# Kernel tuning notes

Measured on AMD Instinct MI355X. Metric: run time of the kernel, lower is better.

Reference implementation:

```python
import jax, jax.numpy as jnp
import numpy as np

B, L, D, N_ITEMS = 512, 100, 128, 100000
ALPHA = 0.3


def setup_inputs() -> dict:
    key = jax.random.key(0)
    ks = jax.random.split(key, 10)
    x = jax.random.randint(ks[0], (B, L), 0, N_ITEMS, dtype=jnp.int32)
    attn_mask = jnp.ones((B, L), dtype=bool)  # unused by forward (parity with torch signature)
    emb = jax.random.normal(ks[1], (N_ITEMS, D), dtype=jnp.float32) * 0.02
    emb = emb.at[0].set(0.0)  # padding_idx=0 row is zeros
    s = 1.0 / np.sqrt(D)
    W_in = jax.random.uniform(ks[2], (D, D), minval=-s, maxval=s, dtype=jnp.float32)
    W_out = jax.random.uniform(ks[3], (D, D), minval=-s, maxval=s, dtype=jnp.float32)
    w_ih = jax.random.uniform(ks[4], (3 * D, D), minval=-s, maxval=s, dtype=jnp.float32)
    w_hh = jax.random.uniform(ks[5], (3 * D, D), minval=-s, maxval=s, dtype=jnp.float32)
    b_ih = jax.random.uniform(ks[6], (3 * D,), minval=-s, maxval=s, dtype=jnp.float32)
    b_hh = jax.random.uniform(ks[7], (3 * D,), minval=-s, maxval=s, dtype=jnp.float32)
    sr = 1.0 / np.sqrt(3 * D)
    W_read = jax.random.uniform(ks[8], (D, 3 * D), minval=-sr, maxval=sr, dtype=jnp.float32)
    b_read = jax.random.uniform(ks[9], (D,), minval=-sr, maxval=sr, dtype=jnp.float32)
    return dict(x=x, attn_mask=attn_mask, emb=emb, W_in=W_in, W_out=W_out,
                w_ih=w_ih, w_hh=w_hh, b_ih=b_ih, b_hh=b_hh, W_read=W_read, b_read=b_read)


def _forward(x, emb, W_in, W_out, w_ih, w_hh, b_ih, b_hh, W_read, b_read):
    n_items, d = emb.shape
    seq_len = x.shape[1]
    BIG = n_items  # sentinel > any item id
    NEG = -1e9

    def per_sample(seq):
        valid = seq != 0
        cnt = valid.sum()
        # --- torch.unique(nonzero, return_inverse=True) via sort + dedup ---
        s = jnp.where(valid, seq, BIG)
        ss = jnp.sort(s)
        prev = jnp.concatenate([jnp.full((1,), -1, ss.dtype), ss[:-1]])
        is_first = (ss != prev) & (ss != BIG)
        n_nodes = is_first.sum()
        rank = jnp.cumsum(is_first) - 1
        nodes_s = jnp.full((seq_len,), BIG, ss.dtype).at[
            jnp.where(is_first, rank, seq_len)].set(ss, mode='drop')  # sorted unique ids, BIG-padded
        node_mask = jnp.arange(seq_len) < n_nodes
        nodes = jnp.where(node_mask, nodes_s, 0)  # pad slots -> item 0 (zero emb row)
        inv = jnp.searchsorted(nodes_s, s)  # inverse indices for valid positions
        # compact nonzero items preserving order (for consecutive-pair edges)
        pos = jnp.cumsum(valid) - 1
        cidx = jnp.where(valid, pos, seq_len)
        compact_inv = jnp.zeros((seq_len,), inv.dtype).at[cidx].set(inv, mode='drop')
        compact_seq = jnp.zeros((seq_len,), seq.dtype).at[cidx].set(seq, mode='drop')
        last_tok = compact_seq[jnp.maximum(cnt - 1, 0)]
        src, dst = compact_inv[:-1], compact_inv[1:]
        edge_mask = jnp.arange(seq_len - 1) < cnt - 1
        # --- message passing: index_add + degree normalize ---
        H0 = emb[nodes]  # [L, d]
        Hin = H0 @ W_in.T
        Hout = H0 @ W_out.T
        dst_safe = jnp.where(edge_mask, dst, seq_len)
        agg = jnp.zeros((seq_len, d), H0.dtype).at[dst_safe].add(
            jnp.where(edge_mask[:, None], Hout[src], 0.0), mode='drop')
        deg = jnp.zeros((seq_len,), H0.dtype).at[dst_safe].add(1.0, mode='drop')
        deg = jnp.maximum(deg, 1.0)
        xin = Hin + agg / deg[:, None]
        # --- GRUCell(xin, H0), torch gate order (r, z, n) ---
        gi = xin @ w_ih.T + b_ih
        gh = H0 @ w_hh.T + b_hh
        gi_r, gi_z, gi_n = jnp.split(gi, 3, axis=-1)
        gh_r, gh_z, gh_n = jnp.split(gh, 3, axis=-1)
        r = jax.nn.sigmoid(gi_r + gh_r)
        z = jax.nn.sigmoid(gi_z + gh_z)
        nct = jnp.tanh(gi_n + r * gh_n)
        H = (1.0 - z) * nct + z * H0
        H = jnp.where(node_mask[:, None], H, 0.0)  # drop padded node slots
        # --- attention readout anchored at last item ---
        li = jnp.clip(jnp.searchsorted(nodes_s, last_tok), 0, seq_len - 1)
        h_last = H[li]
        scores = jnp.where(node_mask, H @ h_last, NEG)
        att = jax.nn.softmax(scores)
        local = att @ H
        gvec = jnp.zeros((d,), H.dtype)  # cooc is None -> zeros_like(local)
        h_read = jnp.tanh(W_read @ jnp.concatenate([h_last, local, ALPHA * gvec]) + b_read)
        row = h_read @ emb.T  # tied output weights
        default = jnp.full((n_items,), NEG, row.dtype).at[0].set(0.0)
        return jnp.where(cnt >= 2, row, default)

    return jax.vmap(per_sample)(x)


def reference(x, attn_mask, emb, W_in, W_out, w_ih, w_hh, b_ih, b_hh, W_read, b_read):
    return _forward(x, emb, W_in, W_out, w_ih, w_hh, b_ih, b_hh, W_read, b_read)
```

## Files before the change

kernel.cpp:

```cpp
#include <hip/hip_runtime.h>
#include <math.h>

#define BATCH 512
#define SEQL  100
#define DIM   128
#define NITEMS 100000
#define NEGV  -1000000000.0f

#define OFF_WREADT 131072
#define OFF_HREAD  180224
#define OFF_DEG    245760
#define OFF_XIN    296960
#define OFF_HOUT   6850560
#define OFF_EPACK_F (OFF_XIN + 131072)
#define OFF_NODES_I 13404160
#define OFF_SRC_I   13455360
#define OFF_DST_I   13506048
#define OFF_INFO_I  13556736
#define OFF_WPACK_F 13558784

typedef __attribute__((ext_vector_type(8))) short bf16x8;
typedef __attribute__((ext_vector_type(4))) short s16x4;
typedef __attribute__((ext_vector_type(4))) float f32x4;

__device__ __forceinline__ unsigned short bf16_rne(float x) {
  unsigned int u = __float_as_uint(x);
  unsigned int r = u + 0x7FFFu + ((u >> 16) & 1u);
  return (unsigned short)(r >> 16);
}
__device__ __forceinline__ float bf16_to_f(unsigned short h) {
  return __uint_as_float(((unsigned int)h) << 16);
}

__global__ void k_prep(const float* __restrict__ w_ih, const float* __restrict__ w_hh,
                       const float* __restrict__ W_in, const float* __restrict__ W_out,
                       const float* __restrict__ W_read, float* __restrict__ ws,
                       unsigned short* __restrict__ wpack) {
  int idx = blockIdx.x * 256 + threadIdx.x;
  if (idx < 98304) {
    int mat = idx / 49152, rem = idx % 49152;
    int n = rem / 128, k = rem % 128;
    float v = (mat ? w_hh : w_ih)[rem];
    unsigned short hi = bf16_rne(v);
    unsigned short lo = bf16_rne(v - bf16_to_f(hi));
    int nt = n >> 4, nn = n & 15, c = k >> 5, quad = (k >> 3) & 3, j = k & 7;
    int lane = quad * 16 + nn;
    size_t base = ((size_t)((mat * 24 + nt) * 4 + c)) * 1024 + (size_t)lane * 8 + j;
    wpack[base] = hi;
    wpack[base + 512] = lo;
  }
  if (idx < 49152) {
    int i = idx / 384, jj = idx % 384;
    ws[OFF_WREADT + jj * 128 + i] = W_read[idx];
  }
  if (idx < 32768) {
    int mat = idx >> 14, rem = idx & 16383;
    int n = rem >> 7, k = rem & 127;
    float v = (mat ? W_out : W_in)[rem];
    unsigned short hi = bf16_rne(v);
    unsigned short lo = bf16_rne(v - bf16_to_f(hi));
    int nt = n >> 4, nn = n & 15, c = k >> 5, quad = (k >> 3) & 3, j = k & 7;
    int lane = quad * 16 + nn;
    size_t base = ((size_t)((mat * 8 + nt) * 4 + c)) * 1024 + (size_t)lane * 8 + j;
    unsigned short* wpack2 = (unsigned short*)ws;
    wpack2[base] = hi;
    wpack2[base + 512] = lo;
  }
}

__global__ void k_build(const int* __restrict__ x, int* __restrict__ nodes,
                        float* __restrict__ deg, int* __restrict__ esrc,
                        int* __restrict__ edst, int* __restrict__ info) {
  int b = blockIdx.x, tid = threadIdx.x;
  __shared__ int sseq[SEQL];
  __shared__ int sfo[SEQL];
  __shared__ unsigned char sisf[SEQL];
  __shared__ int srank[SEQL];
  __shared__ int spos[SEQL];
  __shared__ int scinv[SEQL];
  __shared__ float sdeg[SEQL];
  __shared__ int s_nn, s_cnt;

  if (tid < SEQL) sseq[tid] = x[b * SEQL + tid];
  __syncthreads();
  int t = (tid < SEQL) ? sseq[tid] : 0;
  bool valid = (tid < SEQL) && (t != 0);
  int f = tid;
  if (valid) {
    for (int j = 0; j < tid; ++j) {
      if (sseq[j] == t) { f = j; break; }
    }
  }
  if (tid < SEQL) {
    sfo[tid] = f;
    sisf[tid] = (valid && f == tid) ? 1 : 0;
    sdeg[tid] = 0.f;
  }
  __syncthreads();
  if (tid == 0) {
    int nn = 0, c = 0;
    for (int i = 0; i < SEQL; ++i) {
      srank[i] = nn; nn += sisf[i];
      spos[i] = c;  c += (sseq[i] != 0) ? 1 : 0;
    }
    s_nn = nn; s_cnt = c;
  }
  __syncthreads();
  int nn = s_nn, cnt = s_cnt;
  if (valid) scinv[spos[tid]] = srank[sfo[tid]];
  __syncthreads();
  if (tid < SEQL) {
    if (sisf[tid]) nodes[b * SEQL + srank[tid]] = t;
    if (tid >= nn) nodes[b * SEQL + tid] = 0;
  }
  __syncthreads();
  if (tid == 0) {
    int ec = (cnt >= 2) ? cnt - 1 : 0;
    for (int e = 0; e < ec; ++e) {
      int s = scinv[e], dnode = scinv[e + 1];
      esrc[b * 99 + e] = s;
      edst[b * 99 + e] = dnode;
      sdeg[dnode] += 1.f;
    }
    info[b * 4 + 0] = ec;
    info[b * 4 + 1] = (cnt >= 1) ? scinv[cnt - 1] : 0;
    info[b * 4 + 2] = (cnt >= 2) ? 1 : 0;
    info[b * 4 + 3] = nn;
  }
  __syncthreads();
  if (tid < SEQL) deg[b * SEQL + tid] = fmaxf(sdeg[tid], 1.f);
}

#define GPAD 136
__global__ __launch_bounds__(128) void k_gemm_inout(
    const float* __restrict__ emb, const unsigned short* __restrict__ wpack2,
    const int* __restrict__ nodes, float* __restrict__ xin, float* __restrict__ hout) {
  __shared__ unsigned short Hhi[32 * GPAD];
  __shared__ unsigned short Hlo[32 * GPAD];
  int tid = threadIdx.x;
  int rowbase = blockIdx.x * 32;
  const float4* emb4 = (const float4*)emb;
  for (int e = tid; e < 32 * 32; e += 128) {
    int r = e >> 5, c4 = e & 31;
    int tok = nodes[rowbase + r];
    float4 hv = emb4[(size_t)tok * 32 + c4];
    int base = r * GPAD + c4 * 4;
    float hs[4] = {hv.x, hv.y, hv.z, hv.w};
    #pragma unroll
    for (int q = 0; q < 4; ++q) {
      unsigned short hh = bf16_rne(hs[q]);
      Hhi[base + q] = hh;
      Hlo[base + q] = bf16_rne(hs[q] - bf16_to_f(hh));
    }
  }
  __syncthreads();
  int wave = tid >> 6, lane = tid & 63;
  int quad = lane >> 4, nIdx = lane & 15;
  int mrow = wave * 16 + nIdx;
  bf16x8 aH[4], aL[4];
  #pragma unroll
  for (int c = 0; c < 4; ++c) {
    int off = mrow * GPAD + c * 32 + quad * 8;
    aH[c] = *(const bf16x8*)&Hhi[off];
    aL[c] = *(const bf16x8*)&Hlo[off];
  }
  for (int t = 0; t < 8; ++t) {
    f32x4 accI = (f32x4){0.f, 0.f, 0.f, 0.f};
    f32x4 accO = (f32x4){0.f, 0.f, 0.f, 0.f};
    #pragma unroll
    for (int c = 0; c < 4; ++c) {
      size_t bi = ((size_t)((0 * 8 + t) * 4 + c)) * 1024 + (size_t)lane * 8;
      size_t bo = ((size_t)((1 * 8 + t) * 4 + c)) * 1024 + (size_t)lane * 8;
      bf16x8 BiH = *(const bf16x8*)&wpack2[bi];
      bf16x8 BiL = *(const bf16x8*)&wpack2[bi + 512];
      bf16x8 BoH = *(const bf16x8*)&wpack2[bo];
      bf16x8 BoL = *(const bf16x8*)&wpack2[bo + 512];
      accI = __builtin_amdgcn_mfma_f32_16x16x32_bf16(aH[c], BiH, accI, 0, 0, 0);
      accO = __builtin_amdgcn_mfma_f32_16x16x32_bf16(aH[c], BoH, accO, 0, 0, 0);
      accI = __builtin_amdgcn_mfma_f32_16x16x32_bf16(aL[c], BiH, accI, 0, 0, 0);
      accO = __builtin_amdgcn_mfma_f32_16x16x32_bf16(aL[c], BoH, accO, 0, 0, 0);
      accI = __builtin_amdgcn_mfma_f32_16x16x32_bf16(aH[c], BiL, accI, 0, 0, 0);
      accO = __builtin_amdgcn_mfma_f32_16x16x32_bf16(aH[c], BoL, accO, 0, 0, 0);
    }
    int j = t * 16 + nIdx;
    #pragma unroll
    for (int i = 0; i < 4; ++i) {
      size_t row = (size_t)(rowbase + wave * 16 + quad * 4 + i);
      xin[row * 128 + j]  = accI[i];
      hout[row * 128 + j] = accO[i];
    }
  }
}

__global__ void k_scatter(const float* __restrict__ hout, float* __restrict__ xin,
                          const float* __restrict__ deg, const int* __restrict__ esrc,
                          const int* __restrict__ edst, const int* __restrict__ info) {
  int b = blockIdx.x, k = threadIdx.x;
  __shared__ float agg[SEQL * DIM];
  for (int n = 0; n < SEQL; ++n) agg[n * DIM + k] = 0.f;
  int ec = info[b * 4 + 0];
  for (int e = 0; e < ec; ++e) {
    int s = esrc[b * 99 + e], dn = edst[b * 99 + e];
    agg[dn * DIM + k] += hout[((size_t)(b * SEQL + s)) * DIM + k];
  }
  for (int n = 0; n < SEQL; ++n) {
    float dg = deg[b * SEQL + n];
    size_t idx = ((size_t)(b * SEQL + n)) * DIM + k;
    xin[idx] += agg[n * DIM + k] / dg;
  }
}

__global__ __launch_bounds__(128) void k_gru(
    const float* __restrict__ emb, const int* __restrict__ nodes,
    const unsigned short* __restrict__ wpack, const float* __restrict__ xin,
    const float* __restrict__ b_ih, const float* __restrict__ b_hh,
    const int* __restrict__ info, float* __restrict__ Hbuf) {
  __shared__ unsigned short Xhi[32 * GPAD];
  __shared__ unsigned short Xlo[32 * GPAD];
  __shared__ unsigned short Hhi[32 * GPAD];
  __shared__ unsigned short Hlo[32 * GPAD];
  int tid = threadIdx.x;
  int rowbase = blockIdx.x * 32;
  const float4* emb4 = (const float4*)emb;
  const float4* xin4 = (const float4*)xin;
  for (int e = tid; e < 32 * 32; e += 128) {
    int r = e >> 5, c4 = e & 31;
    int row = rowbase + r;
    float4 xv = xin4[(size_t)row * 32 + c4];
    int tok = nodes[row];
    float4 hv = emb4[(size_t)tok * 32 + c4];
    int base = r * GPAD + c4 * 4;
    float xs[4] = {xv.x, xv.y, xv.z, xv.w};
    float hs[4] = {hv.x, hv.y, hv.z, hv.w};
    #pragma unroll
    for (int q = 0; q < 4; ++q) {
      unsigned short xh = bf16_rne(xs[q]);
      Xhi[base + q] = xh; Xlo[base + q] = bf16_rne(xs[q] - bf16_to_f(xh));
      unsigned short hh = bf16_rne(hs[q]);
      Hhi[base + q] = hh; Hlo[base + q] = bf16_rne(hs[q] - bf16_to_f(hh));
    }
  }
  __syncthreads();
  int wave = tid >> 6, lane = tid & 63;
  int quad = lane >> 4, nIdx = lane & 15;
  int mrow = wave * 16 + nIdx;
  bf16x8 aXh[4], aXl[4], aHh[4], aHl[4];
  #pragma unroll
  for (int c = 0; c < 4; ++c) {
    int off = mrow * GPAD + c * 32 + quad * 8;
    aXh[c] = *(const bf16x8*)&Xhi[off];
    aXl[c] = *(const bf16x8*)&Xlo[off];
    aHh[c] = *(const bf16x8*)&Hhi[off];
    aHl[c] = *(const bf16x8*)&Hlo[off];
  }
  int grows[4]; int zm[4];
  #pragma unroll
  for (int i = 0; i < 4; ++i) {
    int grow = rowbase + wave * 16 + quad * 4 + i;
    grows[i] = grow;
    int bs = grow / SEQL;
    int n = grow - bs * SEQL;
    zm[i] = (n < info[bs * 4 + 3]) ? 1 : 0;
  }

  for (int t = 0; t < 8; ++t) {
    f32x4 acc[3][2];
    #pragma unroll
    for (int g = 0; g < 3; ++g)
      #pragma unroll
      for (int m = 0; m < 2; ++m) acc[g][m] = (f32x4){0.f, 0.f, 0.f, 0.f};

    for (int c = 0; c < 4; ++c) {
      bf16x8 Bh[3][2], Bl[3][2];
      #pragma unroll
      for (int g = 0; g < 3; ++g) {
        int nt = g * 8 + t;
        #pragma unroll
        for (int m = 0; m < 2; ++m) {
          size_t bidx = (size_t)((m * 24 + nt) * 4 + c) * 1024 + (size_t)lane * 8;
          Bh[g][m] = *(const bf16x8*)&wpack[bidx];
          Bl[g][m] = *(const bf16x8*)&wpack[bidx + 512];
        }
      }
      #pragma unroll
      for (int g = 0; g < 3; ++g) {
        acc[g][0] = __builtin_amdgcn_mfma_f32_16x16x32_bf16(aXh[c], Bh[g][0], acc[g][0], 0, 0, 0);
        acc[g][1] = __builtin_amdgcn_mfma_f32_16x16x32_bf16(aHh[c], Bh[g][1], acc[g][1], 0, 0, 0);
      }
      #pragma unroll
      for (int g = 0; g < 3; ++g) {
        acc[g][0] = __builtin_amdgcn_mfma_f32_16x16x32_bf16(aXh[c], Bl[g][0], acc[g][0], 0, 0, 0);
        acc[g][1] = __builtin_amdgcn_mfma_f32_16x16x32_bf16(aHh[c], Bl[g][1], acc[g][1], 0, 0, 0);
      }
      #pragma unroll
      for (int g = 0; g < 3; ++g) {
        acc[g][0] = __builtin_amdgcn_mfma_f32_16x16x32_bf16(aXl[c], Bh[g][0], acc[g][0], 0, 0, 0);
        acc[g][1] = __builtin_amdgcn_mfma_f32_16x16x32_bf16(aHl[c], Bh[g][1], acc[g][1], 0, 0, 0);
      }
    }
    int j = t * 16 + nIdx;
    float biR = b_ih[j],       bhR = b_hh[j];
    float biZ = b_ih[128 + j], bhZ = b_hh[128 + j];
    float biN = b_ih[256 + j], bhN = b_hh[256 + j];
    #pragma unroll
    for (int i = 0; i < 4; ++i) {
      float gr = acc[0][0][i] + biR + acc[0][1][i] + bhR;
      float gz = acc[1][0][i] + biZ + acc[1][1][i] + bhZ;
      float r = 1.f / (1.f + expf(-gr));
      float z = 1.f / (1.f + expf(-gz));
      float nct = tanhf(acc[2][0][i] + biN + r * (acc[2][1][i] + bhN));
      int lrow = wave * 16 + quad * 4 + i;
      float h0 = bf16_to_f(Hhi[lrow * GPAD + j]) + bf16_to_f(Hlo[lrow * GPAD + j]);
      float h = (1.f - z) * nct + z * h0;
      if (!zm[i]) h = 0.f;
      Hbuf[(size_t)grows[i] * 128 + j] = h;
    }
  }
}

#define HLS 129
__global__ void k_attn(const float* __restrict__ Hbuf, const float* __restrict__ ws,
                       const float* __restrict__ b_read, const int* __restrict__ info,
                       float* __restrict__ hread) {
  int b = blockIdx.x, tid = threadIdx.x;
  __shared__ float Hl[SEQL * HLS];
  __shared__ float sc[128];
  __shared__ float hl[128];
  __shared__ float att[SEQL];
  __shared__ float loc[128];
  __shared__ float redm[2], reds[2];
  int nn = info[b * 4 + 3], li = info[b * 4 + 1];
  for (int e = tid; e < SEQL * 128; e += 128) {
    int r = e >> 7, k = e & 127;
    Hl[r * HLS + k] = Hbuf[((size_t)(b * SEQL + r)) * DIM + k];
  }
  __syncthreads();
  hl[tid] = Hl[li * HLS + tid];
  __syncthreads();
  float scr = NEGV;
  if (tid < nn) {
    float s = 0.f;
    for (int k = 0; k < 128; ++k) s += Hl[tid * HLS + k] * hl[k];
    scr = s;
  }
  sc[tid] = scr;
  __syncthreads();
  float m = sc[tid];
  #pragma unroll
  for (int o = 32; o >= 1; o >>= 1) m = fmaxf(m, __shfl_xor(m, o, 64));
  if ((tid & 63) == 0) redm[tid >> 6] = m;
  __syncthreads();
  m = fmaxf(redm[0], redm[1]);
  float e = (tid < SEQL) ? expf(sc[tid] - m) : 0.f;
  float s = e;
  #pragma unroll
  for (int o = 32; o >= 1; o >>= 1) s += __shfl_xor(s, o, 64);
  if ((tid & 63) == 0) reds[tid >> 6] = s;
  __syncthreads();
  float inv = 1.f / (reds[0] + reds[1]);
  if (tid < SEQL) att[tid] = e * inv;
  __syncthreads();
  float lv = 0.f;
  for (int n = 0; n < SEQL; ++n) lv = fmaf(att[n], Hl[n * HLS + tid], lv);
  loc[tid] = lv;
  __syncthreads();
  const float* WrT = ws + OFF_WREADT;
  float acc = b_read[tid];
  for (int j = 0; j < 128; ++j) acc = fmaf(WrT[j * 128 + tid], hl[j], acc);
  for (int j = 0; j < 128; ++j) acc = fmaf(WrT[(128 + j) * 128 + tid], loc[j], acc);
  hread[b * 128 + tid] = tanhf(acc);
}

__global__ __launch_bounds__(256) void k_packA(
    const float* __restrict__ hread, unsigned short* __restrict__ apack) {
  int idx = blockIdx.x * 256 + threadIdx.x;
  if (idx >= 8192) return;
  int lane = idx & 63;
  int kc = (idx >> 6) & 3;
  int mt = idx >> 8;
  int quad = lane >> 4, rr = lane & 15;
  int row = mt * 16 + rr;
  int kbase = kc * 32 + quad * 8;
  const float4* hr4 = (const float4*)(hread + row * 128 + kbase);
  float4 v0 = hr4[0], v1 = hr4[1];
  float vs[8] = {v0.x, v0.y, v0.z, v0.w, v1.x, v1.y, v1.z, v1.w};
  bf16x8 hi, lo;
  #pragma unroll
  for (int j = 0; j < 8; ++j) {
    unsigned short h = bf16_rne(vs[j]);
    hi[j] = (short)h;
    lo[j] = (short)bf16_rne(vs[j] - bf16_to_f(h));
  }
  size_t base = ((size_t)(mt * 4 + kc) * 2) * 512 + (size_t)lane * 8;
  *(bf16x8*)&apack[base] = hi;
  *(bf16x8*)&apack[base + 512] = lo;
}

__global__ __launch_bounds__(256) void k_epack(
    const float* __restrict__ emb, unsigned short* __restrict__ epack) {
  int idx = blockIdx.x * 256 + threadIdx.x;
  int lane = idx & 63;
  int kc = (idx >> 6) & 3;
  int it = idx >> 8;
  int quad = lane >> 4, rr = lane & 15;
  int row = it * 16 + rr;
  int kbase = kc * 32 + quad * 8;
  float4 v0 = {0.f, 0.f, 0.f, 0.f}, v1 = {0.f, 0.f, 0.f, 0.f};
  if (row < NITEMS) {
    const float4* p = (const float4*)(emb + (size_t)row * 128 + kbase);
    v0 = p[0]; v1 = p[1];
  }
  float vs[8] = {v0.x, v0.y, v0.z, v0.w, v1.x, v1.y, v1.z, v1.w};
  bf16x8 hi, lo;
  #pragma unroll
  for (int j = 0; j < 8; ++j) {
    unsigned short h = bf16_rne(vs[j]);
    hi[j] = (short)h;
    lo[j] = (short)bf16_rne(vs[j] - bf16_to_f(h));
  }
  size_t base = ((size_t)(it * 4 + kc) * 2) * 512 + (size_t)lane * 8;
  *(bf16x8*)&epack[base] = hi;
  *(bf16x8*)&epack[base + 512] = lo;
}

__global__ __launch_bounds__(256) void k_out(
    const unsigned short* __restrict__ epack, const unsigned short* __restrict__ apack,
    const int* __restrict__ info, float* __restrict__ out) {
  int tid = threadIdx.x;
  int wave = tid >> 6, lane = tid & 63;
  int quad = lane >> 4, nIdx = lane & 15;
  int b0   = blockIdx.x * 128;
  int itt0 = blockIdx.y * 4;
  int btg0 = blockIdx.x * 8 + wave * 2;

  bf16x8 bh[2][4], bl[2][4];
  #pragma unroll
  for (int m2 = 0; m2 < 2; ++m2)
    #pragma unroll
    for (int kc = 0; kc < 4; ++kc) {
      size_t base = ((size_t)((btg0 + m2) * 4 + kc) * 2) * 512 + (size_t)lane * 8;
      bh[m2][kc] = *(const bf16x8*)&apack[base];
      bl[m2][kc] = *(const bf16x8*)&apack[base + 512];
    }

  f32x4 acc[4][2];
  #pragma unroll
  for (int it = 0; it < 4; ++it)
    #pragma unroll
    for (int m2 = 0; m2 < 2; ++m2) acc[it][m2] = (f32x4){0.f, 0.f, 0.f, 0.f};

  #pragma unroll
  for (int it = 0; it < 4; ++it) {
    #pragma unroll
    for (int kc = 0; kc < 4; ++kc) {
      size_t abase = ((size_t)((itt0 + it) * 4 + kc) * 2) * 512 + (size_t)lane * 8;
      bf16x8 Ah = *(const bf16x8*)&epack[abase];
      bf16x8 Al = *(const bf16x8*)&epack[abase + 512];
      acc[it][0] = __builtin_amdgcn_mfma_f32_16x16x32_bf16(Ah, bh[0][kc], acc[it][0], 0, 0, 0);
      acc[it][1] = __builtin_amdgcn_mfma_f32_16x16x32_bf16(Ah, bh[1][kc], acc[it][1], 0, 0, 0);
      acc[it][0] = __builtin_amdgcn_mfma_f32_16x16x32_bf16(Al, bh[0][kc], acc[it][0], 0, 0, 0);
      acc[it][1] = __builtin_amdgcn_mfma_f32_16x16x32_bf16(Al, bh[1][kc], acc[it][1], 0, 0, 0);
      acc[it][0] = __builtin_amdgcn_mfma_f32_16x16x32_bf16(Ah, bl[0][kc], acc[it][0], 0, 0, 0);
      acc[it][1] = __builtin_amdgcn_mfma_f32_16x16x32_bf16(Ah, bl[1][kc], acc[it][1], 0, 0, 0);
    }
  }

  #pragma unroll
  for (int m2 = 0; m2 < 2; ++m2) {
    int b = b0 + (wave * 2 + m2) * 16 + nIdx;
    int flag = info[b * 4 + 2];
    #pragma unroll
    for (int it = 0; it < 4; ++it) {
      int ib = (itt0 + it) * 16 + quad * 4;
      if (ib < NITEMS) {
        float4 v;
        if (flag) {
          v.x = acc[it][m2][0]; v.y = acc[it][m2][1];
          v.z = acc[it][m2][2]; v.w = acc[it][m2][3];
        } else {
          v.x = (ib == 0) ? 0.f : NEGV; v.y = NEGV; v.z = NEGV; v.w = NEGV;
        }
        *(float4*)&out[(size_t)b * NITEMS + ib] = v;
      }
    }
  }
}

extern "C" void kernel_launch(void* const* d_in, const int* in_sizes, int n_in,
                              void* d_out, int out_size, void* d_ws, size_t ws_size,
                              hipStream_t stream) {
  const int*   x      = (const int*)d_in[0];
  const float* emb    = (const float*)d_in[2];
  const float* W_in   = (const float*)d_in[3];
  const float* W_out  = (const float*)d_in[4];
  const float* w_ih   = (const float*)d_in[5];
  const float* w_hh   = (const float*)d_in[6];
  const float* b_ih   = (const float*)d_in[7];
  const float* b_hh   = (const float*)d_in[8];
  const float* W_read = (const float*)d_in[9];
  const float* b_read = (const float*)d_in[10];
  float* ws  = (float*)d_ws;
  int*   wsi = (int*)d_ws;
  unsigned short* wpack  = (unsigned short*)(ws + OFF_WPACK_F);
  unsigned short* wpack2 = (unsigned short*)ws;
  unsigned short* apack  = (unsigned short*)(ws + OFF_XIN);
  unsigned short* epack  = (unsigned short*)(ws + OFF_EPACK_F);
  float* out = (float*)d_out;

  k_prep<<<384, 256, 0, stream>>>(w_ih, w_hh, W_in, W_out, W_read, ws, wpack);
  k_build<<<BATCH, 128, 0, stream>>>(x, wsi + OFF_NODES_I, ws + OFF_DEG,
                                     wsi + OFF_SRC_I, wsi + OFF_DST_I, wsi + OFF_INFO_I);
  k_gemm_inout<<<1600, 128, 0, stream>>>(emb, wpack2, wsi + OFF_NODES_I,
                                         ws + OFF_XIN, ws + OFF_HOUT);
  k_scatter<<<BATCH, 128, 0, stream>>>(ws + OFF_HOUT, ws + OFF_XIN, ws + OFF_DEG,
                                       wsi + OFF_SRC_I, wsi + OFF_DST_I, wsi + OFF_INFO_I);
  k_gru<<<1600, 128, 0, stream>>>(emb, wsi + OFF_NODES_I, wpack, ws + OFF_XIN,
                                  b_ih, b_hh, wsi + OFF_INFO_I, ws + OFF_HOUT);
  k_attn<<<BATCH, 128, 0, stream>>>(ws + OFF_HOUT, ws, b_read, wsi + OFF_INFO_I,
                                    ws + OFF_HREAD);
  k_epack<<<6252, 256, 0, stream>>>(emb, epack);
  k_packA<<<32, 256, 0, stream>>>(ws + OFF_HREAD, apack);
  k_out<<<dim3(4, 1563), 256, 0, stream>>>(epack, apack, wsi + OFF_INFO_I, out);
}
```

Measured before the change: 473.5 us.

## Fuse graph build, aggregation and GRU into one per-sample kernel

Measured after the change: 827.0 us. +74.7%, slower.

```diff
diff --git a/kernel.cpp b/kernel.cpp
--- a/kernel.cpp
+++ b/kernel.cpp
@@ -7,17 +7,12 @@
 #define NITEMS 100000
 #define NEGV  -1000000000.0f
 
-#define OFF_WREADT 131072
-#define OFF_HREAD  180224
-#define OFF_DEG    245760
-#define OFF_XIN    296960
-#define OFF_HOUT   6850560
-#define OFF_EPACK_F (OFF_XIN + 131072)
-#define OFF_NODES_I 13404160
-#define OFF_SRC_I   13455360
-#define OFF_DST_I   13506048
-#define OFF_INFO_I  13556736
-#define OFF_WPACK_F 13558784
+#define OFF_WPACK_F 0
+#define OFF_WREADT  147456
+#define OFF_APACK_F 196608
+#define OFF_HBUF    262144
+#define OFF_EPACK_F 6815744
+#define OFF_INFO_I  19619840
 
 typedef __attribute__((ext_vector_type(8))) short bf16x8;
 typedef __attribute__((ext_vector_type(4))) short s16x4;
@@ -32,296 +27,262 @@
   return __uint_as_float(((unsigned int)h) << 16);
 }
 
-__global__ void k_prep(const float* __restrict__ w_ih, const float* __restrict__ w_hh,
-                       const float* __restrict__ W_in, const float* __restrict__ W_out,
-                       const float* __restrict__ W_read, float* __restrict__ ws,
-                       unsigned short* __restrict__ wpack) {
-  int idx = blockIdx.x * 256 + threadIdx.x;
-  if (idx < 98304) {
+__global__ __launch_bounds__(256) void k_pack(
+    const float* __restrict__ emb, const float* __restrict__ w_ih,
+    const float* __restrict__ w_hh, const float* __restrict__ W_in,
+    const float* __restrict__ W_out, const float* __restrict__ W_read,
+    float* __restrict__ WreadT, unsigned short* __restrict__ wpack,
+    unsigned short* __restrict__ epack) {
+  int bid = blockIdx.x, tid = threadIdx.x;
+  if (bid < 6252) {
+    int idx = bid * 256 + tid;
+    int lane = idx & 63;
+    int kc = (idx >> 6) & 3;
+    int it = idx >> 8;
+    int quad = lane >> 4, rr = lane & 15;
+    int row = it * 16 + rr;
+    int kbase = kc * 32 + quad * 8;
+    float4 v0 = {0.f, 0.f, 0.f, 0.f}, v1 = {0.f, 0.f, 0.f, 0.f};
+    if (row < NITEMS) {
+      const float4* p = (const float4*)(emb + (size_t)row * 128 + kbase);
+      v0 = p[0]; v1 = p[1];
+    }
+    float vs[8] = {v0.x, v0.y, v0.z, v0.w, v1.x, v1.y, v1.z, v1.w};
+    bf16x8 hi, lo;
+    #pragma unroll
+    for (int j = 0; j < 8; ++j) {
+      unsigned short h = bf16_rne(vs[j]);
+      hi[j] = (short)h;
+      lo[j] = (short)bf16_rne(vs[j] - bf16_to_f(h));
+    }
+    size_t base = ((size_t)(it * 4 + kc) * 2) * 512 + (size_t)lane * 8;
+    *(bf16x8*)&epack[base] = hi;
+    *(bf16x8*)&epack[base + 512] = lo;
+  } else if (bid < 6828) {
+    int idx = (bid - 6252) * 256 + tid;
     int mat = idx / 49152, rem = idx % 49152;
-    int n = rem / 128, k = rem % 128;
-    float v = (mat ? w_hh : w_ih)[rem];
+    int n = rem >> 7, k = rem & 127;
+    float v;
+    if (mat == 2) {
+      v = w_hh[rem];
+    } else {
+      const float* Wx = mat ? W_out : W_in;
+      const float* wr = w_ih + n * 128;
+      float s = 0.f;
+      for (int m = 0; m < 128; ++m) s = fmaf(wr[m], Wx[m * 128 + k], s);
+      v = s;
+    }
     unsigned short hi = bf16_rne(v);
     unsigned short lo = bf16_rne(v - bf16_to_f(hi));
-    int nt = n >> 4, nn = n & 15, c = k >> 5, quad = (k >> 3) & 3, j = k & 7;
-    int lane = quad * 16 + nn;
+    int nt = n >> 4, nn2 = n & 15, c = k >> 5, quad = (k >> 3) & 3, j = k & 7;
+    int lane = quad * 16 + nn2;
     size_t base = ((size_t)((mat * 24 + nt) * 4 + c)) * 1024 + (size_t)lane * 8 + j;
     wpack[base] = hi;
     wpack[base + 512] = lo;
-  }
-  if (idx < 49152) {
+  } else {
+    int idx = (bid - 6828) * 256 + tid;
     int i = idx / 384, jj = idx % 384;
-    ws[OFF_WREADT + jj * 128 + i] = W_read[idx];
-  }
-  if (idx < 32768) {
-    int mat = idx >> 14, rem = idx & 16383;
-    int n = rem >> 7, k = rem & 127;
-    float v = (mat ? W_out : W_in)[rem];
-    unsigned short hi = bf16_rne(v);
-    unsigned short lo = bf16_rne(v - bf16_to_f(hi));
-    int nt = n >> 4, nn = n & 15, c = k >> 5, quad = (k >> 3) & 3, j = k & 7;
-    int lane = quad * 16 + nn;
-    size_t base = ((size_t)((mat * 8 + nt) * 4 + c)) * 1024 + (size_t)lane * 8 + j;
-    unsigned short* wpack2 = (unsigned short*)ws;
-    wpack2[base] = hi;
-    wpack2[base + 512] = lo;
-  }
-}
-
-__global__ void k_build(const int* __restrict__ x, int* __restrict__ nodes,
-                        float* __restrict__ deg, int* __restrict__ esrc,
-                        int* __restrict__ edst, int* __restrict__ info) {
-  int b = blockIdx.x, tid = threadIdx.x;
+    WreadT[jj * 128 + i] = W_read[idx];
+  }
+}
+
+__global__ __launch_bounds__(512) void k_fused(
+    const int* __restrict__ x, const float* __restrict__ emb,
+    const unsigned short* __restrict__ wpack,
+    const float* __restrict__ b_ih, const float* __restrict__ b_hh,
+    int* __restrict__ info, float* __restrict__ Hbuf) {
+  __shared__ unsigned short H0s[2 * 112 * 136];
+  __shared__ float Gmem[15232];
+  __shared__ unsigned short Bst[2 * 9216];
   __shared__ int sseq[SEQL];
-  __shared__ int sfo[SEQL];
   __shared__ unsigned char sisf[SEQL];
   __shared__ int srank[SEQL];
-  __shared__ int spos[SEQL];
   __shared__ int scinv[SEQL];
-  __shared__ float sdeg[SEQL];
+  __shared__ int snodes[112];
+  __shared__ float sdeg[112];
   __shared__ int s_nn, s_cnt;
+  int b = blockIdx.x, tid = threadIdx.x;
 
   if (tid < SEQL) sseq[tid] = x[b * SEQL + tid];
+  if (tid < 112) { snodes[tid] = 0; sdeg[tid] = 0.f; }
   __syncthreads();
   int t = (tid < SEQL) ? sseq[tid] : 0;
   bool valid = (tid < SEQL) && (t != 0);
   int f = tid;
   if (valid) {
-    for (int j = 0; j < tid; ++j) {
-      if (sseq[j] == t) { f = j; break; }
-    }
-  }
+    for (int j = 0; j < tid; ++j) if (sseq[j] == t) { f = j; break; }
+  }
+  int isf = (valid && f == tid) ? 1 : 0;
+  if (tid < SEQL) sisf[tid] = (unsigned char)isf;
+  __syncthreads();
+  int rank = 0, pos = 0;
   if (tid < SEQL) {
-    sfo[tid] = f;
-    sisf[tid] = (valid && f == tid) ? 1 : 0;
-    sdeg[tid] = 0.f;
-  }
-  __syncthreads();
+    for (int i = 0; i < tid; ++i) {
+      rank += sisf[i];
+      pos += (sseq[i] != 0) ? 1 : 0;
+    }
+    srank[tid] = rank;
+    if (tid == SEQL - 1) { s_nn = rank + isf; s_cnt = pos + (valid ? 1 : 0); }
+  }
+  __syncthreads();
+  if (valid) scinv[pos] = srank[f];
+  if (isf) snodes[rank] = t;
+  __syncthreads();
+  int nn = s_nn, cnt = s_cnt;
+  int ec = (cnt >= 2) ? cnt - 1 : 0;
+  if (tid < ec) atomicAdd(&sdeg[scinv[tid + 1]], 1.f);
   if (tid == 0) {
-    int nn = 0, c = 0;
-    for (int i = 0; i < SEQL; ++i) {
-      srank[i] = nn; nn += sisf[i];
-      spos[i] = c;  c += (sseq[i] != 0) ? 1 : 0;
-    }
-    s_nn = nn; s_cnt = c;
-  }
-  __syncthreads();
-  int nn = s_nn, cnt = s_cnt;
-  if (valid) scinv[spos[tid]] = srank[sfo[tid]];
-  __syncthreads();
-  if (tid < SEQL) {
-    if (sisf[tid]) nodes[b * SEQL + srank[tid]] = t;
-    if (tid >= nn) nodes[b * SEQL + tid] = 0;
-  }
-  __syncthreads();
-  if (tid == 0) {
-    int ec = (cnt >= 2) ? cnt - 1 : 0;
-    for (int e = 0; e < ec; ++e) {
-      int s = scinv[e], dnode = scinv[e + 1];
-      esrc[b * 99 + e] = s;
-      edst[b * 99 + e] = dnode;
-      sdeg[dnode] += 1.f;
-    }
     info[b * 4 + 0] = ec;
     info[b * 4 + 1] = (cnt >= 1) ? scinv[cnt - 1] : 0;
     info[b * 4 + 2] = (cnt >= 2) ? 1 : 0;
     info[b * 4 + 3] = nn;
   }
-  __syncthreads();
-  if (tid < SEQL) deg[b * SEQL + tid] = fmaxf(sdeg[tid], 1.f);
-}
-
-#define GPAD 136
-__global__ __launch_bounds__(128) void k_gemm_inout(
-    const float* __restrict__ emb, const unsigned short* __restrict__ wpack2,
-    const int* __restrict__ nodes, float* __restrict__ xin, float* __restrict__ hout) {
-  __shared__ unsigned short Hhi[32 * GPAD];
-  __shared__ unsigned short Hlo[32 * GPAD];
-  int tid = threadIdx.x;
-  int rowbase = blockIdx.x * 32;
   const float4* emb4 = (const float4*)emb;
-  for (int e = tid; e < 32 * 32; e += 128) {
+  for (int e = tid; e < 112 * 32; e += 512) {
     int r = e >> 5, c4 = e & 31;
-    int tok = nodes[rowbase + r];
-    float4 hv = emb4[(size_t)tok * 32 + c4];
-    int base = r * GPAD + c4 * 4;
-    float hs[4] = {hv.x, hv.y, hv.z, hv.w};
+    float4 v = emb4[(size_t)snodes[r] * 32 + c4];
+    float vs[4] = {v.x, v.y, v.z, v.w};
+    s16x4 hv, lv;
     #pragma unroll
     for (int q = 0; q < 4; ++q) {
-      unsigned short hh = bf16_rne(hs[q]);
-      Hhi[base + q] = hh;
-      Hlo[base + q] = bf16_rne(hs[q] - bf16_to_f(hh));
-    }
-  }
-  __syncthreads();
-  int wave = tid >> 6, lane = tid & 63;
+      unsigned short h = bf16_rne(vs[q]);
+      hv[q] = (short)h;
+      lv[q] = (short)bf16_rne(vs[q] - bf16_to_f(h));
+    }
+    *(s16x4*)&H0s[r * 136 + c4 * 4] = hv;
+    *(s16x4*)&H0s[112 * 136 + r * 136 + c4 * 4] = lv;
+  }
+  float4* G4 = (float4*)Gmem;
+  for (int e = tid; e < 112 * 33; e += 512) G4[e] = (float4){0.f, 0.f, 0.f, 0.f};
+  __syncthreads();
+  for (int idx = tid; idx < ec * 128; idx += 512) {
+    int e = idx >> 7, k = idx & 127;
+    int src = scinv[e], dst = scinv[e + 1];
+    float v = bf16_to_f(H0s[src * 136 + k]) + bf16_to_f(H0s[112 * 136 + src * 136 + k]);
+    atomicAdd(&Gmem[dst * 132 + k], v);
+  }
+  __syncthreads();
+  float sv[28];
+  #pragma unroll
+  for (int u = 0; u < 28; ++u) {
+    int e = tid + u * 512;
+    int r = e >> 7, k = e & 127;
+    sv[u] = Gmem[r * 132 + k] * (1.f / fmaxf(sdeg[r], 1.f));
+  }
+  __syncthreads();
+  unsigned short* GdU = (unsigned short*)Gmem;
+  #pragma unroll
+  for (int u = 0; u < 28; ++u) {
+    int e = tid + u * 512;
+    int r = e >> 7, k = e & 127;
+    unsigned short hi = bf16_rne(sv[u]);
+    GdU[r * 136 + k] = hi;
+    GdU[112 * 136 + r * 136 + k] = bf16_rne(sv[u] - bf16_to_f(hi));
+  }
+  __syncthreads();
+
+  int w = tid >> 6, lane = tid & 63;
   int quad = lane >> 4, nIdx = lane & 15;
-  int mrow = wave * 16 + nIdx;
-  bf16x8 aH[4], aL[4];
-  #pragma unroll
-  for (int c = 0; c < 4; ++c) {
-    int off = mrow * GPAD + c * 32 + quad * 8;
-    aH[c] = *(const bf16x8*)&Hhi[off];
-    aL[c] = *(const bf16x8*)&Hlo[off];
-  }
-  for (int t = 0; t < 8; ++t) {
-    f32x4 accI = (f32x4){0.f, 0.f, 0.f, 0.f};
-    f32x4 accO = (f32x4){0.f, 0.f, 0.f, 0.f};
+  const uint4* wp4 = (const uint4*)wpack;
+  uint4* bst4 = (uint4*)Bst;
+
+  bf16x8 a0h[4], a0l[4], a1h[4], a1l[4];
+  if (w < 7) {
     #pragma unroll
     for (int c = 0; c < 4; ++c) {
-      size_t bi = ((size_t)((0 * 8 + t) * 4 + c)) * 1024 + (size_t)lane * 8;
-      size_t bo = ((size_t)((1 * 8 + t) * 4 + c)) * 1024 + (size_t)lane * 8;
-      bf16x8 BiH = *(const bf16x8*)&wpack2[bi];
-      bf16x8 BiL = *(const bf16x8*)&wpack2[bi + 512];
-      bf16x8 BoH = *(const bf16x8*)&wpack2[bo];
-      bf16x8 BoL = *(const bf16x8*)&wpack2[bo + 512];
-      accI = __builtin_amdgcn_mfma_f32_16x16x32_bf16(aH[c], BiH, accI, 0, 0, 0);
-      accO = __builtin_amdgcn_mfma_f32_16x16x32_bf16(aH[c], BoH, accO, 0, 0, 0);
-      accI = __builtin_amdgcn_mfma_f32_16x16x32_bf16(aL[c], BiH, accI, 0, 0, 0);
-      accO = __builtin_amdgcn_mfma_f32_16x16x32_bf16(aL[c], BoH, accO, 0, 0, 0);
-      accI = __builtin_amdgcn_mfma_f32_16x16x32_bf16(aH[c], BiL, accI, 0, 0, 0);
-      accO = __builtin_amdgcn_mfma_f32_16x16x32_bf16(aH[c], BoL, accO, 0, 0, 0);
-    }
-    int j = t * 16 + nIdx;
-    #pragma unroll
-    for (int i = 0; i < 4; ++i) {
-      size_t row = (size_t)(rowbase + wave * 16 + quad * 4 + i);
-      xin[row * 128 + j]  = accI[i];
-      hout[row * 128 + j] = accO[i];
-    }
-  }
-}
-
-__global__ void k_scatter(const float* __restrict__ hout, float* __restrict__ xin,
-                          const float* __restrict__ deg, const int* __restrict__ esrc,
-                          const int* __restrict__ edst, const int* __restrict__ info) {
-  int b = blockIdx.x, k = threadIdx.x;
-  __shared__ float agg[SEQL * DIM];
-  for (int n = 0; n < SEQL; ++n) agg[n * DIM + k] = 0.f;
-  int ec = info[b * 4 + 0];
-  for (int e = 0; e < ec; ++e) {
-    int s = esrc[b * 99 + e], dn = edst[b * 99 + e];
-    agg[dn * DIM + k] += hout[((size_t)(b * SEQL + s)) * DIM + k];
-  }
-  for (int n = 0; n < SEQL; ++n) {
-    float dg = deg[b * SEQL + n];
-    size_t idx = ((size_t)(b * SEQL + n)) * DIM + k;
-    xin[idx] += agg[n * DIM + k] / dg;
-  }
-}
-
-__global__ __launch_bounds__(128) void k_gru(
-    const float* __restrict__ emb, const int* __restrict__ nodes,
-    const unsigned short* __restrict__ wpack, const float* __restrict__ xin,
-    const float* __restrict__ b_ih, const float* __restrict__ b_hh,
-    const int* __restrict__ info, float* __restrict__ Hbuf) {
-  __shared__ unsigned short Xhi[32 * GPAD];
-  __shared__ unsigned short Xlo[32 * GPAD];
-  __shared__ unsigned short Hhi[32 * GPAD];
-  __shared__ unsigned short Hlo[32 * GPAD];
-  int tid = threadIdx.x;
-  int rowbase = blockIdx.x * 32;
-  const float4* emb4 = (const float4*)emb;
-  const float4* xin4 = (const float4*)xin;
-  for (int e = tid; e < 32 * 32; e += 128) {
-    int r = e >> 5, c4 = e & 31;
-    int row = rowbase + r;
-    float4 xv = xin4[(size_t)row * 32 + c4];
-    int tok = nodes[row];
-    float4 hv = emb4[(size_t)tok * 32 + c4];
-    int base = r * GPAD + c4 * 4;
-    float xs[4] = {xv.x, xv.y, xv.z, xv.w};
-    float hs[4] = {hv.x, hv.y, hv.z, hv.w};
-    #pragma unroll
-    for (int q = 0; q < 4; ++q) {
-      unsigned short xh = bf16_rne(xs[q]);
-      Xhi[base + q] = xh; Xlo[base + q] = bf16_rne(xs[q] - bf16_to_f(xh));
-      unsigned short hh = bf16_rne(hs[q]);
-      Hhi[base + q] = hh; Hlo[base + q] = bf16_rne(hs[q] - bf16_to_f(hh));
-    }
-  }
-  __syncthreads();
-  int wave = tid >> 6, lane = tid & 63;
-  int quad = lane >> 4, nIdx = lane & 15;
-  int mrow = wave * 16 + nIdx;
-  bf16x8 aXh[4], aXl[4], aHh[4], aHl[4];
-  #pragma unroll
-  for (int c = 0; c < 4; ++c) {
-    int off = mrow * GPAD + c * 32 + quad * 8;
-    aXh[c] = *(const bf16x8*)&Xhi[off];
-    aXl[c] = *(const bf16x8*)&Xlo[off];
-    aHh[c] = *(const bf16x8*)&Hhi[off];
-    aHl[c] = *(const bf16x8*)&Hlo[off];
-  }
-  int grows[4]; int zm[4];
-  #pragma unroll
-  for (int i = 0; i < 4; ++i) {
-    int grow = rowbase + wave * 16 + quad * 4 + i;
-    grows[i] = grow;
-    int bs = grow / SEQL;
-    int n = grow - bs * SEQL;
-    zm[i] = (n < info[bs * 4 + 3]) ? 1 : 0;
-  }
-
-  for (int t = 0; t < 8; ++t) {
-    f32x4 acc[3][2];
-    #pragma unroll
-    for (int g = 0; g < 3; ++g)
+      int aoff = (w * 16 + nIdx) * 136 + c * 32 + quad * 8;
+      a0h[c] = *(const bf16x8*)&H0s[aoff];
+      a0l[c] = *(const bf16x8*)&H0s[112 * 136 + aoff];
+      a1h[c] = *(const bf16x8*)&GdU[aoff];
+      a1l[c] = *(const bf16x8*)&GdU[112 * 136 + aoff];
+    }
+  }
+  #define STAGE(S, BS)                                                         \
+    {                                                                          \
+      int tts = (S) >> 2, cs = (S) & 3;                                        \
+      for (int u = tid; u < 1152; u += 512) {                                  \
+        int ch = u >> 7, off = u & 127;                                        \
+        int g = ch / 3, mat = ch - 3 * g;                                      \
+        bst4[(BS) * 1152 + ch * 128 + off] =                                   \
+            wp4[((mat * 24 + g * 8 + tts) * 4 + cs) * 128 + off];              \
+      }                                                                        \
+    }
+  STAGE(0, 0)
+  __syncthreads();
+
+  f32x4 acc[3][2];
+  for (int s = 0; s < 32; ++s) {
+    int bs = s & 1;
+    if (s + 1 < 32) STAGE(s + 1, bs ^ 1)
+    int tt = s >> 2, c = s & 3;
+    if (w < 7) {
+      if (c == 0) {
+        #pragma unroll
+        for (int g = 0; g < 3; ++g)
+          #pragma unroll
+          for (int m = 0; m < 2; ++m) acc[g][m] = (f32x4){0.f, 0.f, 0.f, 0.f};
+      }
+      bf16x8 Bh[3][3], Bl[3][3];
       #pragma unroll
-      for (int m = 0; m < 2; ++m) acc[g][m] = (f32x4){0.f, 0.f, 0.f, 0.f};
-
-    for (int c = 0; c < 4; ++c) {
-      bf16x8 Bh[3][2], Bl[3][2];
+      for (int g = 0; g < 3; ++g)
+        #pragma unroll
+        for (int mat = 0; mat < 3; ++mat) {
+          int boff = bs * 9216 + (g * 3 + mat) * 1024 + lane * 8;
+          Bh[g][mat] = *(const bf16x8*)&Bst[boff];
+          Bl[g][mat] = *(const bf16x8*)&Bst[boff + 512];
+        }
       #pragma unroll
       for (int g = 0; g < 3; ++g) {
-        int nt = g * 8 + t;
-        #pragma unroll
-        for (int m = 0; m < 2; ++m) {
-          size_t bidx = (size_t)((m * 24 + nt) * 4 + c) * 1024 + (size_t)lane * 8;
-          Bh[g][m] = *(const bf16x8*)&wpack[bidx];
-          Bl[g][m] = *(const bf16x8*)&wpack[bidx + 512];
-        }
+        acc[g][0] = __builtin_amdgcn_mfma_f32_16x16x32_bf16(a0h[c], Bh[g][0], acc[g][0], 0, 0, 0);
+        acc[g][1] = __builtin_amdgcn_mfma_f32_16x16x32_bf16(a0h[c], Bh[g][2], acc[g][1], 0, 0, 0);
       }
       #pragma unroll
       for (int g = 0; g < 3; ++g) {
-        acc[g][0] = __builtin_amdgcn_mfma_f32_16x16x32_bf16(aXh[c], Bh[g][0], acc[g][0], 0, 0, 0);
-        acc[g][1] = __builtin_amdgcn_mfma_f32_16x16x32_bf16(aHh[c], Bh[g][1], acc[g][1], 0, 0, 0);
+        acc[g][0] = __builtin_amdgcn_mfma_f32_16x16x32_bf16(a1h[c], Bh[g][1], acc[g][0], 0, 0, 0);
+        acc[g][1] = __builtin_amdgcn_mfma_f32_16x16x32_bf16(a0l[c], Bh[g][2], acc[g][1], 0, 0, 0);
       }
       #pragma unroll
       for (int g = 0; g < 3; ++g) {
-        acc[g][0] = __builtin_amdgcn_mfma_f32_16x16x32_bf16(aXh[c], Bl[g][0], acc[g][0], 0, 0, 0);
-        acc[g][1] = __builtin_amdgcn_mfma_f32_16x16x32_bf16(aHh[c], Bl[g][1], acc[g][1], 0, 0, 0);
+        acc[g][0] = __builtin_amdgcn_mfma_f32_16x16x32_bf16(a0l[c], Bh[g][0], acc[g][0], 0, 0, 0);
+        acc[g][1] = __builtin_amdgcn_mfma_f32_16x16x32_bf16(a0h[c], Bl[g][2], acc[g][1], 0, 0, 0);
       }
       #pragma unroll
       for (int g = 0; g < 3; ++g) {
-        acc[g][0] = __builtin_amdgcn_mfma_f32_16x16x32_bf16(aXl[c], Bh[g][0], acc[g][0], 0, 0, 0);
-        acc[g][1] = __builtin_amdgcn_mfma_f32_16x16x32_bf16(aHl[c], Bh[g][1], acc[g][1], 0, 0, 0);
-      }
-    }
-    int j = t * 16 + nIdx;
-    float biR = b_ih[j],       bhR = b_hh[j];
-    float biZ = b_ih[128 + j], bhZ = b_hh[128 + j];
-    float biN = b_ih[256 + j], bhN = b_hh[256 + j];
-    #pragma unroll
-    for (int i = 0; i < 4; ++i) {
-      float gr = acc[0][0][i] + biR + acc[0][1][i] + bhR;
-      float gz = acc[1][0][i] + biZ + acc[1][1][i] + bhZ;
-      float r = 1.f / (1.f + expf(-gr));
-      float z = 1.f / (1.f + expf(-gz));
-      float nct = tanhf(acc[2][0][i] + biN + r * (acc[2][1][i] + bhN));
-      int lrow = wave * 16 + quad * 4 + i;
-      float h0 = bf16_to_f(Hhi[lrow * GPAD + j]) + bf16_to_f(Hlo[lrow * GPAD + j]);
-      float h = (1.f - z) * nct + z * h0;
-      if (!zm[i]) h = 0.f;
-      Hbuf[(size_t)grows[i] * 128 + j] = h;
-    }
-  }
+        acc[g][0] = __builtin_amdgcn_mfma_f32_16x16x32_bf16(a1l[c], Bh[g][1], acc[g][0], 0, 0, 0);
+        acc[g][0] = __builtin_amdgcn_mfma_f32_16x16x32_bf16(a0h[c], Bl[g][0], acc[g][0], 0, 0, 0);
+        acc[g][0] = __builtin_amdgcn_mfma_f32_16x16x32_bf16(a1h[c], Bl[g][1], acc[g][0], 0, 0, 0);
+      }
+      if (c == 3) {
+        int j = tt * 16 + nIdx;
+        float biR = b_ih[j],       bhR = b_hh[j];
+        float biZ = b_ih[128 + j], bhZ = b_hh[128 + j];
+        float biN = b_ih[256 + j], bhN = b_hh[256 + j];
+        #pragma unroll
+        for (int i = 0; i < 4; ++i) {
+          int row = w * 16 + quad * 4 + i;
+          if (row < SEQL) {
+            float gr = acc[0][0][i] + biR + acc[0][1][i] + bhR;
+            float gz = acc[1][0][i] + biZ + acc[1][1][i] + bhZ;
+            float r = 1.f / (1.f + expf(-gr));
+            float z = 1.f / (1.f + expf(-gz));
+            float nct = tanhf(acc[2][0][i] + biN + r * (acc[2][1][i] + bhN));
+            float h0 = bf16_to_f(H0s[row * 136 + j]) + bf16_to_f(H0s[112 * 136 + row * 136 + j]);
+            float h = (1.f - z) * nct + z * h0;
+            if (row >= nn) h = 0.f;
+            Hbuf[((size_t)b * SEQL + row) * 128 + j] = h;
+          }
+        }
+      }
+    }
+    __syncthreads();
+  }
+  #undef STAGE
 }
 
 #define HLS 129
-__global__ void k_attn(const float* __restrict__ Hbuf, const float* __restrict__ ws,
+__global__ void k_attn(const float* __restrict__ Hbuf, const float* __restrict__ WrT,
                        const float* __restrict__ b_read, const int* __restrict__ info,
-                       float* __restrict__ hread) {
+                       unsigned short* __restrict__ apack) {
   int b = blockIdx.x, tid = threadIdx.x;
   __shared__ float Hl[SEQL * HLS];
   __shared__ float sc[128];
@@ -364,63 +325,17 @@
   for (int n = 0; n < SEQL; ++n) lv = fmaf(att[n], Hl[n * HLS + tid], lv);
   loc[tid] = lv;
   __syncthreads();
-  const float* WrT = ws + OFF_WREADT;
   float acc = b_read[tid];
   for (int j = 0; j < 128; ++j) acc = fmaf(WrT[j * 128 + tid], hl[j], acc);
   for (int j = 0; j < 128; ++j) acc = fmaf(WrT[(128 + j) * 128 + tid], loc[j], acc);
-  hread[b * 128 + tid] = tanhf(acc);
-}
-
-__global__ __launch_bounds__(256) void k_packA(
-    const float* __restrict__ hread, unsigned short* __restrict__ apack) {
-  int idx = blockIdx.x * 256 + threadIdx.x;
-  if (idx >= 8192) return;
-  int lane = idx & 63;
-  int kc = (idx >> 6) & 3;
-  int mt = idx >> 8;
-  int quad = lane >> 4, rr = lane & 15;
-  int row = mt * 16 + rr;
-  int kbase = kc * 32 + quad * 8;
-  const float4* hr4 = (const float4*)(hread + row * 128 + kbase);
-  float4 v0 = hr4[0], v1 = hr4[1];
-  float vs[8] = {v0.x, v0.y, v0.z, v0.w, v1.x, v1.y, v1.z, v1.w};
-  bf16x8 hi, lo;
-  #pragma unroll
-  for (int j = 0; j < 8; ++j) {
-    unsigned short h = bf16_rne(vs[j]);
-    hi[j] = (short)h;
-    lo[j] = (short)bf16_rne(vs[j] - bf16_to_f(h));
-  }
-  size_t base = ((size_t)(mt * 4 + kc) * 2) * 512 + (size_t)lane * 8;
-  *(bf16x8*)&apack[base] = hi;
-  *(bf16x8*)&apack[base + 512] = lo;
-}
-
-__global__ __launch_bounds__(256) void k_epack(
-    const float* __restrict__ emb, unsigned short* __restrict__ epack) {
-  int idx = blockIdx.x * 256 + threadIdx.x;
-  int lane = idx & 63;
-  int kc = (idx >> 6) & 3;
-  int it = idx >> 8;
-  int quad = lane >> 4, rr = lane & 15;
-  int row = it * 16 + rr;
-  int kbase = kc * 32 + quad * 8;
-  float4 v0 = {0.f, 0.f, 0.f, 0.f}, v1 = {0.f, 0.f, 0.f, 0.f};
-  if (row < NITEMS) {
-    const float4* p = (const float4*)(emb + (size_t)row * 128 + kbase);
-    v0 = p[0]; v1 = p[1];
-  }
-  float vs[8] = {v0.x, v0.y, v0.z, v0.w, v1.x, v1.y, v1.z, v1.w};
-  bf16x8 hi, lo;
-  #pragma unroll
-  for (int j = 0; j < 8; ++j) {
-    unsigned short h = bf16_rne(vs[j]);
-    hi[j] = (short)h;
-    lo[j] = (short)bf16_rne(vs[j] - bf16_to_f(h));
-  }
-  size_t base = ((size_t)(it * 4 + kc) * 2) * 512 + (size_t)lane * 8;
-  *(bf16x8*)&epack[base] = hi;
-  *(bf16x8*)&epack[base + 512] = lo;
+  float hr = tanhf(acc);
+  int mt = b >> 4, rr = b & 15;
+  int kc = tid >> 5, q2 = (tid >> 3) & 3, j2 = tid & 7;
+  unsigned short hi = bf16_rne(hr);
+  unsigned short lo = bf16_rne(hr - bf16_to_f(hi));
+  size_t base = ((size_t)(mt * 4 + kc) * 2) * 512 + (size_t)(q2 * 16 + rr) * 8 + j2;
+  apack[base] = hi;
+  apack[base + 512] = lo;
 }
 
 __global__ __launch_bounds__(256) void k_out(
@@ -501,24 +416,17 @@
   const float* b_read = (const float*)d_in[10];
   float* ws  = (float*)d_ws;
   int*   wsi = (int*)d_ws;
-  unsigned short* wpack  = (unsigned short*)(ws + OFF_WPACK_F);
-  unsigned short* wpack2 = (unsigned short*)ws;
-  unsigned short* apack  = (unsigned short*)(ws + OFF_XIN);
-  unsigned short* epack  = (unsigned short*)(ws + OFF_EPACK_F);
+  unsigned short* wpack = (unsigned short*)(ws + OFF_WPACK_F);
+  float*          WreadT = ws + OFF_WREADT;
+  unsigned short* apack = (unsigned short*)(ws + OFF_APACK_F);
+  float*          Hbuf  = ws + OFF_HBUF;
+  unsigned short* epack = (unsigned short*)(ws + OFF_EPACK_F);
+  int*            info  = wsi + OFF_INFO_I;
   float* out = (float*)d_out;
 
-  k_prep<<<384, 256, 0, stream>>>(w_ih, w_hh, W_in, W_out, W_read, ws, wpack);
-  k_build<<<BATCH, 128, 0, stream>>>(x, wsi + OFF_NODES_I, ws + OFF_DEG,
-                                     wsi + OFF_SRC_I, wsi + OFF_DST_I, wsi + OFF_INFO_I);
-  k_gemm_inout<<<1600, 128, 0, stream>>>(emb, wpack2, wsi + OFF_NODES_I,
-                                         ws + OFF_XIN, ws + OFF_HOUT);
-  k_scatter<<<BATCH, 128, 0, stream>>>(ws + OFF_HOUT, ws + OFF_XIN, ws + OFF_DEG,
-                                       wsi + OFF_SRC_I, wsi + OFF_DST_I, wsi + OFF_INFO_I);
-  k_gru<<<1600, 128, 0, stream>>>(emb, wsi + OFF_NODES_I, wpack, ws + OFF_XIN,
-                                  b_ih, b_hh, wsi + OFF_INFO_I, ws + OFF_HOUT);
-  k_attn<<<BATCH, 128, 0, stream>>>(ws + OFF_HOUT, ws, b_read, wsi + OFF_INFO_I,
-                                    ws + OFF_HREAD);
-  k_epack<<<6252, 256, 0, stream>>>(emb, epack);
-  k_packA<<<32, 256, 0, stream>>>(ws + OFF_HREAD, apack);
-  k_out<<<dim3(4, 1563), 256, 0, stream>>>(epack, apack, wsi + OFF_INFO_I, out);
-}
+  k_pack<<<7020, 256, 0, stream>>>(emb, w_ih, w_hh, W_in, W_out, W_read,
+                                   WreadT, wpack, epack);
+  k_fused<<<BATCH, 512, 0, stream>>>(x, emb, wpack, b_ih, b_hh, info, Hbuf);
+  k_attn<<<BATCH, 128, 0, stream>>>(Hbuf, WreadT, b_read, info, apack);
+  k_out<<<dim3(4, 1563), 256, 0, stream>>>(epack, apack, info, out);
+}
```
